# Kernel tuning notes

Measured on AMD Instinct MI355X. Metric: run time of the kernel, lower is better.

Reference implementation:

```python
import jax, jax.numpy as jnp
import numpy as np

NQ = 8
DEPTH = 2

def _apply_1q(state, U, q):
    # state: (B, 2,...,2); U: (2,2) shared or (B,2,2) per-sample; acts on qubit q
    s = jnp.moveaxis(state, 1 + q, -1)
    if U.ndim == 3:
        s = jnp.einsum('bij,b...j->b...i', U, s)
    else:
        s = jnp.einsum('ij,...j->...i', U, s)
    return jnp.moveaxis(s, -1, 1 + q)

def _cnot(state, c, t):
    s = jnp.moveaxis(state, (1 + c, 1 + t), (-2, -1))
    s = jnp.concatenate([s[..., :1, :], s[..., 1:, ::-1]], axis=-2)
    return jnp.moveaxis(s, (-2, -1), (1 + c, 1 + t))

def _rx(t):
    c = jnp.cos(t / 2).astype(jnp.complex64)
    s = (-1j * jnp.sin(t / 2)).astype(jnp.complex64)
    return jnp.stack([jnp.stack([c, s]), jnp.stack([s, c])])

def _ry(t):
    c = jnp.cos(t / 2)
    s = jnp.sin(t / 2)
    return jnp.stack([jnp.stack([c, -s]), jnp.stack([s, c])]).astype(jnp.complex64)

def _rz(t):
    e = jnp.exp(-1j * t / 2).astype(jnp.complex64)
    z = jnp.zeros((), jnp.complex64)
    return jnp.stack([jnp.stack([e, z]), jnp.stack([z, jnp.conj(e)])])

def _simulate(qparams, angles):
    # Batched 8-qubit state-vector simulator replacing the per-sample PennyLane loop.
    # angles: (B, NQ) encoding angles. qparams: (DEPTH, NQ, 3).
    B = angles.shape[0]
    state = jnp.zeros((B,) + (2,) * NQ, jnp.complex64)
    state = state.at[(slice(None),) + (0,) * NQ].set(1.0 + 0j)
    # data encoding: per-sample RX(angles[:, q]) on qubit q
    for q in range(NQ):
        t = angles[:, q]
        c = jnp.cos(t / 2).astype(jnp.complex64)
        s = (-1j * jnp.sin(t / 2)).astype(jnp.complex64)
        U = jnp.stack([jnp.stack([c, s], -1), jnp.stack([s, c], -1)], -2)  # (B,2,2)
        state = _apply_1q(state, U, q)
    for layer in range(DEPTH):
        for q in range(NQ):
            state = _apply_1q(state, _rx(qparams[layer, q, 0]), q)
            state = _apply_1q(state, _ry(qparams[layer, q, 1]), q)
            state = _apply_1q(state, _rz(qparams[layer, q, 2]), q)
        for q in range(NQ - 1):
            state = _cnot(state, q, q + 1)
    probs = state.real ** 2 + state.imag ** 2  # (B, 2,...,2)
    outs = []
    for q in range(NQ):
        axes = tuple(a for a in range(1, NQ + 1) if a != 1 + q)
        m = probs.sum(axes)  # (B, 2)
        outs.append(m[:, 0] - m[:, 1])  # <Z_q>
    return jnp.stack(outs, axis=1).astype(jnp.float32)

def _leaky(x):
    return jnp.where(x >= 0, x, 0.2 * x)

def setup_inputs():
    key = jax.random.key(0)
    k = jax.random.split(key, 16)
    B, IMG, H, NC = 4096, 128, 256, 6
    D = IMG * IMG
    def w(kk, o, i):
        return (jax.random.normal(kk, (o, i), jnp.float32) / np.float32(np.sqrt(i)))
    return {
        'img': jax.random.normal(k[0], (B, 1, IMG, IMG), jnp.float32),
        'class_id': jax.random.randint(k[1], (B,), 0, NC),
        'W1': w(k[2], H, D), 'b1': jnp.zeros((H,), jnp.float32),
        'W2': w(k[3], H, H), 'b2': jnp.zeros((H,), jnp.float32),
        'W3': w(k[4], NQ, H), 'b3': jnp.zeros((NQ,), jnp.float32),
        'qparams': jax.random.normal(k[5], (DEPTH, NQ, 3), jnp.float32),
        'emb': jax.random.normal(k[6], (NC, NC), jnp.float32),
        'W4': w(k[7], H, NQ + NC), 'b4': jnp.zeros((H,), jnp.float32),
        'W5': w(k[8], H // 2, H), 'b5': jnp.zeros((H // 2,), jnp.float32),
        'W6': w(k[9], 1, H // 2), 'b6': jnp.zeros((1,), jnp.float32),
    }

def reference(img, class_id, W1, b1, W2, b2, W3, b3, qparams, emb, W4, b4, W5, b5, W6, b6):
    B = img.shape[0]
    x = img.reshape(B, -1)
    h = _leaky(x @ W1.T + b1)
    h = _leaky(h @ W2.T + b2)
    q_in = h @ W3.T + b3  # (B, NQ)
    angles = (q_in + 1.0) * np.float32(np.pi / 2)
    # torch code wraps circuit output in torch.tensor(...) -> detached
    qf = jax.lax.stop_gradient(_simulate(qparams, angles))
    ce = emb[class_id]
    comb = jnp.concatenate([qf, ce], axis=1)
    h = _leaky(comb @ W4.T + b4)
    h = _leaky(h @ W5.T + b5)
    return h @ W6.T + b6
```

## Files before the change

### kernel.cpp

```cpp
#include <hip/hip_runtime.h>
#include <hip/hip_bf16.h>

#define B_SZ 4096
#define DDIM 16384
#define HDIM 256
#define NQ 8

typedef __attribute__((ext_vector_type(8))) short bf16x8;
typedef __attribute__((ext_vector_type(4))) short s16x4;
typedef __attribute__((ext_vector_type(4))) float f32x4;
typedef unsigned int u32;

__device__ inline short f2bf(float f) {
    union { float f; unsigned u; } v; v.f = f;
    unsigned r = v.u + 0x7fffu + ((v.u >> 16) & 1u);
    return (short)(r >> 16);
}
__device__ inline float bf2f(short h) {
    union { unsigned u; float f; } v; v.u = ((unsigned)(unsigned short)h) << 16;
    return v.f;
}
__device__ inline float lrelu(float x) { return x >= 0.f ? x : 0.2f * x; }

__device__ inline float2 cmul(float2 a, float2 b) {
    return make_float2(a.x * b.x - a.y * b.y, a.x * b.y + a.y * b.x);
}
__device__ inline float2 cadd(float2 a, float2 b) {
    return make_float2(a.x + b.x, a.y + b.y);
}

__device__ inline void async16(void* lds, const void* g) {
    __builtin_amdgcn_global_load_lds(
        (const __attribute__((address_space(1))) u32*)g,
        (__attribute__((address_space(3))) u32*)lds, 16, 0, 0);
}

__device__ inline void mk_hilo(float4 a, float4 b, bf16x8& hi, bf16x8& lo) {
    float xs[8] = {a.x, a.y, a.z, a.w, b.x, b.y, b.z, b.w};
#pragma unroll
    for (int j = 0; j < 8; j++) {
        short h = f2bf(xs[j]);
        hi[j] = h;
        lo[j] = f2bf(xs[j] - bf2f(h));
    }
}

__global__ __launch_bounds__(256) void convW(
    const float* __restrict__ W1, const float* __restrict__ W2,
    const float* __restrict__ W4, const float* __restrict__ W5,
    const float* __restrict__ qp,
    char* __restrict__ W1s, char* __restrict__ W2s,
    short* __restrict__ W4h, short* __restrict__ W4l,
    short* __restrict__ W5h, short* __restrict__ W5l,
    float* __restrict__ Umat)
{
    const int bid = blockIdx.x, t = threadIdx.x;
    if (bid < 4096) {
        int idx = bid * 256 + t;
        int r = idx >> 12, cg = idx & 4095;
        int kb = cg >> 4, c4 = cg & 15;
        float4 v = *(const float4*)(W1 + ((size_t)idx << 2));
        s16x4 h = (s16x4){f2bf(v.x), f2bf(v.y), f2bf(v.z), f2bf(v.w)};
        int byte = (r * 128 + c4 * 8) ^ ((r & 7) << 4);
        *(s16x4*)(W1s + kb * 32768 + byte) = h;
    } else if (bid < 4160) {
        int idx = (bid - 4096) * 256 + t;
        int r = idx >> 6, cg = idx & 63;
        int kb = cg >> 4, c4 = cg & 15;
        float4 v = *(const float4*)(W2 + ((size_t)idx << 2));
        s16x4 h = (s16x4){f2bf(v.x), f2bf(v.y), f2bf(v.z), f2bf(v.w)};
        int byte = (r * 128 + c4 * 8) ^ ((r & 7) << 4);
        *(s16x4*)(W2s + kb * 32768 + byte) = h;
    } else if (bid < 4192) {
        int idx = (bid - 4160) * 256 + t;
        float4 v = *(const float4*)(W5 + ((size_t)idx << 2));
        float xs[4] = {v.x, v.y, v.z, v.w};
        s16x4 hi, lo;
#pragma unroll
        for (int j = 0; j < 4; j++) {
            short h = f2bf(xs[j]);
            hi[j] = h;
            lo[j] = f2bf(xs[j] - bf2f(h));
        }
        *(s16x4*)(W5h + (size_t)idx * 4) = hi;
        *(s16x4*)(W5l + (size_t)idx * 4) = lo;
    } else {
        const float* wr = W4 + t * 14;
        short* dh = W4h + t * 32;
        short* dl = W4l + t * 32;
#pragma unroll
        for (int j = 0; j < 14; j++) {
            float x = wr[j];
            short h = f2bf(x);
            dh[j] = h;
            dl[j] = f2bf(x - bf2f(h));
        }
#pragma unroll
        for (int j = 14; j < 32; j++) { dh[j] = 0; dl[j] = 0; }
        if (t < 16) {
            float ax = qp[t * 3 + 0], ay = qp[t * 3 + 1], az = qp[t * 3 + 2];
            float sa, ca, sb, cb, sg, cg;
            sincosf(ax * 0.5f, &sa, &ca);
            sincosf(ay * 0.5f, &sb, &cb);
            sincosf(az * 0.5f, &sg, &cg);
            float2 M00 = make_float2(cb * ca,  sb * sa);
            float2 M01 = make_float2(-sb * ca, -cb * sa);
            float2 M10 = make_float2(sb * ca,  -cb * sa);
            float2 M11 = make_float2(cb * ca,  -sb * sa);
            float2 e0 = make_float2(cg, -sg);
            float2 e1 = make_float2(cg,  sg);
            float2* out = (float2*)(Umat + t * 8);
            out[0] = cmul(e0, M00);
            out[1] = cmul(e0, M01);
            out[2] = cmul(e1, M10);
            out[3] = cmul(e1, M11);
        }
    }
}

__global__ __launch_bounds__(512, 2) void gemm1(
    const float* __restrict__ img, const char* __restrict__ W1s,
    float* __restrict__ part)
{
    __shared__ char smem[2][49152];

    const int bid = blockIdx.x;
    const int y = bid & 7, x = bid >> 3;
    const int m0 = x * 128;
    const int t = threadIdx.x, lane = t & 63, w = t >> 6;
    const int arow = t >> 4, ac4 = t & 15;

    f32x4 acc[16];
#pragma unroll
    for (int i = 0; i < 16; i++) acc[i] = (f32x4){0.f, 0.f, 0.f, 0.f};
    float4 ra[4];

    const float* aBase = img + (size_t)m0 * DDIM + y * 2048;
    const char*  bBase = W1s + (size_t)(y * 32) * 32768;

    auto loadA = [&](int it) {
#pragma unroll
        for (int i = 0; i < 4; i++)
            ra[i] = *(const float4*)(aBase + (size_t)(arow + 32 * i) * DDIM + it * 64 + ac4 * 4);
    };
    auto issueB = [&](int it, int buf) {
        const char* src = bBase + it * 32768 + w * 4096 + lane * 16;
        char* dst = &smem[buf][16384 + w * 4096];
#pragma unroll
        for (int i = 0; i < 4; i++)
            async16(dst + i * 1024, src + i * 1024);
    };
    auto writeA = [&](int buf) {
#pragma unroll
        for (int i = 0; i < 4; i++) {
            int row = arow + 32 * i;
            float4 v = ra[i];
            s16x4 h = (s16x4){f2bf(v.x), f2bf(v.y), f2bf(v.z), f2bf(v.w)};
            int byte = (row * 128 + ac4 * 8) ^ ((row & 7) << 4);
            *(s16x4*)(&smem[buf][byte]) = h;
        }
    };
    auto mfma_block = [&](int buf) {
        const char* aT = &smem[buf][0];
        const char* bT = &smem[buf][16384];
#pragma unroll
        for (int ks = 0; ks < 2; ks++) {
            int k0 = ks * 32 + (lane >> 4) * 8;
            int ar = w * 16 + (lane & 15);
            bf16x8 af = *(const bf16x8*)(aT + ((ar * 128 + k0 * 2) ^ ((ar & 7) << 4)));
#pragma unroll
            for (int nf = 0; nf < 16; nf++) {
                int nr = nf * 16 + (lane & 15);
                bf16x8 bfr = *(const bf16x8*)(bT + ((nr * 128 + k0 * 2) ^ ((nr & 7) << 4)));
                acc[nf] = __builtin_amdgcn_mfma_f32_16x16x32_bf16(af, bfr, acc[nf], 0, 0, 0);
            }
        }
    };

    loadA(0);
    issueB(0, 0);
    writeA(0);
    __syncthreads();
    for (int it = 0; it < 32; ++it) {
        int bc = it & 1, bn = bc ^ 1;
        if (it < 31) { loadA(it + 1); issueB(it + 1, bn); }
        mfma_block(bc);
        if (it < 31) writeA(bn);
        __syncthreads();
    }

#pragma unroll
    for (int nf = 0; nf < 16; nf++) {
        int col = nf * 16 + (lane & 15);
#pragma unroll
        for (int r = 0; r < 4; r++) {
            int row = m0 + w * 16 + (lane >> 4) * 4 + r;
            part[((size_t)y * B_SZ + row) * 256 + col] = acc[nf][r];
        }
    }
}

__global__ __launch_bounds__(512) void gemm2(
    const float* __restrict__ part, const char* __restrict__ W2s,
    const float* __restrict__ b1, const float* __restrict__ b2,
    float* __restrict__ h2)
{
    __shared__ char smem[8192 + 32768];
    char* aT = smem;
    char* bT = smem + 8192;

    const int m0 = blockIdx.x * 64;
    const int t = threadIdx.x, lane = t & 63, w = t >> 6;
    const int wq = w & 3, half = w >> 2;

    f32x4 acc[8];
#pragma unroll
    for (int i = 0; i < 8; i++) acc[i] = (f32x4){0.f, 0.f, 0.f, 0.f};

    for (int it = 0; it < 4; ++it) {
        {
            const char* src = W2s + it * 32768 + w * 4096 + lane * 16;
            char* dst = bT + w * 4096;
#pragma unroll
            for (int i = 0; i < 4; i++)
                async16(dst + i * 1024, src + i * 1024);
        }
#pragma unroll
        for (int j = 0; j < 2; j++) {
            int g = t + j * 512;
            int row = g >> 4, c4 = g & 15;
            int kg = it * 64 + c4 * 4;
            float4 s = make_float4(0.f, 0.f, 0.f, 0.f);
#pragma unroll
            for (int yy = 0; yy < 8; yy++) {
                float4 v = *(const float4*)(part + ((size_t)yy * B_SZ + m0 + row) * 256 + kg);
                s.x += v.x; s.y += v.y; s.z += v.z; s.w += v.w;
            }
            float4 bb = *(const float4*)(b1 + kg);
            s.x = lrelu(s.x + bb.x); s.y = lrelu(s.y + bb.y);
            s.z = lrelu(s.z + bb.z); s.w = lrelu(s.w + bb.w);
            s16x4 h = (s16x4){f2bf(s.x), f2bf(s.y), f2bf(s.z), f2bf(s.w)};
            int byte = (row * 128 + c4 * 8) ^ ((row & 7) << 4);
            *(s16x4*)(aT + byte) = h;
        }
        __syncthreads();
#pragma unroll
        for (int ks = 0; ks < 2; ks++) {
            int k0 = ks * 32 + (lane >> 4) * 8;
            int ar = wq * 16 + (lane & 15);
            bf16x8 af = *(const bf16x8*)(aT + ((ar * 128 + k0 * 2) ^ ((ar & 7) << 4)));
#pragma unroll
            for (int nf = 0; nf < 8; nf++) {
                int nr = half * 128 + nf * 16 + (lane & 15);
                bf16x8 bfr = *(const bf16x8*)(bT + ((nr * 128 + k0 * 2) ^ ((nr & 7) << 4)));
                acc[nf] = __builtin_amdgcn_mfma_f32_16x16x32_bf16(af, bfr, acc[nf], 0, 0, 0);
            }
        }
        __syncthreads();
    }

#pragma unroll
    for (int nf = 0; nf < 8; nf++) {
        int col = half * 128 + nf * 16 + (lane & 15);
        float bb = b2[col];
#pragma unroll
        for (int r = 0; r < 4; r++) {
            int row = m0 + wq * 16 + (lane >> 4) * 4 + r;
            h2[(size_t)row * 256 + col] = lrelu(acc[nf][r] + bb);
        }
    }
}

__global__ __launch_bounds__(256) void qsim2(
    const float* __restrict__ h2, const float* __restrict__ W3,
    const float* __restrict__ b3, const float* __restrict__ Ug,
    float* __restrict__ qf)
{
    __shared__ float w3s[8 * 256];
    __shared__ float us[16 * 8];
    __shared__ float b3s[8];
    const int t = threadIdx.x, lane = t & 63, w = t >> 6;

    for (int i = t; i < 2048; i += 256) w3s[i] = W3[i];
    if (t < 128) us[t] = Ug[t];
    if (t < 8) b3s[t] = b3[t];
    __syncthreads();

    const int b = blockIdx.x * 4 + w;
    float4 hv = *(const float4*)(h2 + (size_t)b * 256 + lane * 4);

    float ang[8];
#pragma unroll
    for (int q = 0; q < 8; q++) {
        float4 wv = *(const float4*)(w3s + q * 256 + lane * 4);
        float p = hv.x * wv.x + hv.y * wv.y + hv.z * wv.z + hv.w * wv.w;
#pragma unroll
        for (int m = 1; m < 64; m <<= 1) p += __shfl_xor(p, m, 64);
        ang[q] = (p + b3s[q] + 1.0f) * 0.78539816339744831f;
    }
    float myang = ang[0];
#pragma unroll
    for (int q = 1; q < 8; q++) if (lane == q) myang = ang[q];
    float s_ = 0.f, c_ = 0.f;
    if (lane < 8) sincosf(myang, &s_, &c_);
    float cs[8], sn[8];
#pragma unroll
    for (int q = 0; q < 8; q++) { cs[q] = __shfl(c_, q, 64); sn[q] = __shfl(s_, q, 64); }

    float mL = 1.f;
#pragma unroll
    for (int q = 0; q <= 5; q++) mL *= ((lane >> (5 - q)) & 1) ? sn[q] : cs[q];
    float mg0 = mL * cs[6] * cs[7], mg1 = mL * cs[6] * sn[7];
    float mg2 = mL * sn[6] * cs[7], mg3 = mL * sn[6] * sn[7];
    int pc = __popc(lane);
    auto ph = [](int k, float m) {
        k &= 3;
        if (k == 0) return make_float2(m, 0.f);
        if (k == 1) return make_float2(0.f, -m);
        if (k == 2) return make_float2(-m, 0.f);
        return make_float2(0.f, m);
    };
    float2 a0 = ph(pc, mg0), a1 = ph(pc + 1, mg1), a2 = ph(pc + 1, mg2), a3 = ph(pc + 2, mg3);

#pragma unroll
    for (int l = 0; l < 2; l++) {
#pragma unroll
        for (int q = 0; q < 8; q++) {
            const float* u = us + (l * 8 + q) * 8;
            float2 u00 = make_float2(u[0], u[1]), u01 = make_float2(u[2], u[3]);
            float2 u10 = make_float2(u[4], u[5]), u11 = make_float2(u[6], u[7]);
            if (q <= 5) {
                int sh = 5 - q, msk = 1 << sh, bit = (lane >> sh) & 1;
                float2 ud = bit ? u11 : u00, uo = bit ? u10 : u01;
                float2 p;
                p.x = __shfl_xor(a0.x, msk, 64); p.y = __shfl_xor(a0.y, msk, 64);
                a0 = cadd(cmul(ud, a0), cmul(uo, p));
                p.x = __shfl_xor(a1.x, msk, 64); p.y = __shfl_xor(a1.y, msk, 64);
                a1 = cadd(cmul(ud, a1), cmul(uo, p));
                p.x = __shfl_xor(a2.x, msk, 64); p.y = __shfl_xor(a2.y, msk, 64);
                a2 = cadd(cmul(ud, a2), cmul(uo, p));
                p.x = __shfl_xor(a3.x, msk, 64); p.y = __shfl_xor(a3.y, msk, 64);
                a3 = cadd(cmul(ud, a3), cmul(uo, p));
            } else if (q == 6) {
                float2 n0 = cadd(cmul(u00, a0), cmul(u01, a2));
                float2 n2 = cadd(cmul(u10, a0), cmul(u11, a2));
                float2 n1 = cadd(cmul(u00, a1), cmul(u01, a3));
                float2 n3 = cadd(cmul(u10, a1), cmul(u11, a3));
                a0 = n0; a1 = n1; a2 = n2; a3 = n3;
            } else {
                float2 n0 = cadd(cmul(u00, a0), cmul(u01, a1));
                float2 n1 = cadd(cmul(u10, a0), cmul(u11, a1));
                float2 n2 = cadd(cmul(u00, a2), cmul(u01, a3));
                float2 n3 = cadd(cmul(u10, a2), cmul(u11, a3));
                a0 = n0; a1 = n1; a2 = n2; a3 = n3;
            }
        }
#pragma unroll
        for (int c = 0; c <= 4; c++) {
            int tm = 1 << (4 - c);
            int cb = (lane >> (5 - c)) & 1;
            float2 p;
            p.x = __shfl_xor(a0.x, tm, 64); p.y = __shfl_xor(a0.y, tm, 64);
            if (cb) a0 = p;
            p.x = __shfl_xor(a1.x, tm, 64); p.y = __shfl_xor(a1.y, tm, 64);
            if (cb) a1 = p;
            p.x = __shfl_xor(a2.x, tm, 64); p.y = __shfl_xor(a2.y, tm, 64);
            if (cb) a2 = p;
            p.x = __shfl_xor(a3.x, tm, 64); p.y = __shfl_xor(a3.y, tm, 64);
            if (cb) a3 = p;
        }
        if (lane & 1) { float2 tmp = a0; a0 = a2; a2 = tmp; tmp = a1; a1 = a3; a3 = tmp; }
        { float2 tmp = a2; a2 = a3; a3 = tmp; }
    }

    float p0 = a0.x * a0.x + a0.y * a0.y, p1 = a1.x * a1.x + a1.y * a1.y;
    float p2 = a2.x * a2.x + a2.y * a2.y, p3 = a3.x * a3.x + a3.y * a3.y;
    float S = p0 + p1 + p2 + p3;
    float v0 = ((lane >> 5) & 1) ? -S : S;
    float v1 = ((lane >> 4) & 1) ? -S : S;
    float v2 = ((lane >> 3) & 1) ? -S : S;
    float v3 = ((lane >> 2) & 1) ? -S : S;
    float v4 = ((lane >> 1) & 1) ? -S : S;
    float v5 = (lane & 1) ? -S : S;
    float v6 = p0 + p1 - p2 - p3;
    float v7 = p0 - p1 + p2 - p3;
#pragma unroll
    for (int m = 1; m < 64; m <<= 1) {
        v0 += __shfl_xor(v0, m, 64); v1 += __shfl_xor(v1, m, 64);
        v2 += __shfl_xor(v2, m, 64); v3 += __shfl_xor(v3, m, 64);
        v4 += __shfl_xor(v4, m, 64); v5 += __shfl_xor(v5, m, 64);
        v6 += __shfl_xor(v6, m, 64); v7 += __shfl_xor(v7, m, 64);
    }
    if (lane == 0) {
        float* o = qf + (size_t)b * 8;
        o[0] = v0; o[1] = v1; o[2] = v2; o[3] = v3;
        o[4] = v4; o[5] = v5; o[6] = v6; o[7] = v7;
    }
}

__global__ __launch_bounds__(256) void head_mfma(
    const float* __restrict__ qf, const int* __restrict__ cid,
    const float* __restrict__ emb,
    const short* __restrict__ W4h, const short* __restrict__ W4l,
    const float* __restrict__ b4,
    const short* __restrict__ W5h, const short* __restrict__ W5l,
    const float* __restrict__ b5,
    const float* __restrict__ W6, const float* __restrict__ b6,
    float* __restrict__ out)
{
    __shared__ float comb[64 * 32];
    __shared__ float h3s[64 * 256];
    const int t = threadIdx.x, lane = t & 63, w = t >> 6;
    const int m0 = blockIdx.x * 64;

    if (t < 128) {
        int r = t >> 1, half = t & 1;
        float* d = comb + r * 32;
        if (half == 0) {
            float4 q0 = *(const float4*)(qf + (size_t)(m0 + r) * 8);
            float4 q1 = *(const float4*)(qf + (size_t)(m0 + r) * 8 + 4);
            d[0] = q0.x; d[1] = q0.y; d[2] = q0.z; d[3] = q0.w;
            d[4] = q1.x; d[5] = q1.y; d[6] = q1.z; d[7] = q1.w;
#pragma unroll
            for (int j = 16; j < 24; j++) d[j] = 0.f;
        } else {
            const float* e = emb + cid[m0 + r] * 6;
#pragma unroll
            for (int j = 0; j < 6; j++) d[8 + j] = e[j];
            d[14] = 0.f; d[15] = 0.f;
#pragma unroll
            for (int j = 24; j < 32; j++) d[j] = 0.f;
        }
    }
    __syncthreads();

    f32x4 acc1[16];
#pragma unroll
    for (int i = 0; i < 16; i++) acc1[i] = (f32x4){0.f, 0.f, 0.f, 0.f};
    const int k0 = (lane >> 4) * 8;
    bf16x8 Ahi, Alo;
    {
        const float* p = comb + (w * 16 + (lane & 15)) * 32 + k0;
        mk_hilo(*(const float4*)p, *(const float4*)(p + 4), Ahi, Alo);
    }
#pragma unroll
    for (int nf = 0; nf < 16; nf++) {
        int n = nf * 16 + (lane & 15);
        bf16x8 Bhi = *(const bf16x8*)(W4h + n * 32 + k0);
        bf16x8 Blo = *(const bf16x8*)(W4l + n * 32 + k0);
        acc1[nf] = __builtin_amdgcn_mfma_f32_16x16x32_bf16(Ahi, Bhi, acc1[nf], 0, 0, 0);
        acc1[nf] = __builtin_amdgcn_mfma_f32_16x16x32_bf16(Ahi, Blo, acc1[nf], 0, 0, 0);
        acc1[nf] = __builtin_amdgcn_mfma_f32_16x16x32_bf16(Alo, Bhi, acc1[nf], 0, 0, 0);
    }
#pragma unroll
    for (int nf = 0; nf < 16; nf++) {
        int col = nf * 16 + (lane & 15);
        float bc = b4[col];
#pragma unroll
        for (int r = 0; r < 4; r++) {
            int row = w * 16 + (lane >> 4) * 4 + r;
            float v = lrelu(acc1[nf][r] + bc);
            int byte = row * 1024 + col * 4;
            *(float*)((char*)h3s + (byte ^ ((row & 7) << 4))) = v;
        }
    }
    __syncthreads();

    f32x4 acc2[8];
#pragma unroll
    for (int i = 0; i < 8; i++) acc2[i] = (f32x4){0.f, 0.f, 0.f, 0.f};
#pragma unroll
    for (int ks = 0; ks < 8; ks++) {
        int kf = ks * 32 + (lane >> 4) * 8;
        int row = w * 16 + (lane & 15);
        int base = row * 1024 + kf * 4;
        float4 x0 = *(float4*)((char*)h3s + (base ^ ((row & 7) << 4)));
        float4 x1 = *(float4*)((char*)h3s + ((base + 16) ^ ((row & 7) << 4)));
        bf16x8 Ah, Al;
        mk_hilo(x0, x1, Ah, Al);
#pragma unroll
        for (int nf = 0; nf < 8; nf++) {
            int n = nf * 16 + (lane & 15);
            bf16x8 Bh = *(const bf16x8*)(W5h + n * 256 + kf);
            bf16x8 Bl = *(const bf16x8*)(W5l + n * 256 + kf);
            acc2[nf] = __builtin_amdgcn_mfma_f32_16x16x32_bf16(Ah, Bh, acc2[nf], 0, 0, 0);
            acc2[nf] = __builtin_amdgcn_mfma_f32_16x16x32_bf16(Ah, Bl, acc2[nf], 0, 0, 0);
            acc2[nf] = __builtin_amdgcn_mfma_f32_16x16x32_bf16(Al, Bh, acc2[nf], 0, 0, 0);
        }
    }

    float vs0 = 0.f, vs1 = 0.f, vs2 = 0.f, vs3 = 0.f;
#pragma unroll
    for (int nf = 0; nf < 8; nf++) {
        int col = nf * 16 + (lane & 15);
        float b5c = b5[col], w6c = W6[col];
        vs0 += lrelu(acc2[nf][0] + b5c) * w6c;
        vs1 += lrelu(acc2[nf][1] + b5c) * w6c;
        vs2 += lrelu(acc2[nf][2] + b5c) * w6c;
        vs3 += lrelu(acc2[nf][3] + b5c) * w6c;
    }
#pragma unroll
    for (int m = 1; m < 16; m <<= 1) {
        vs0 += __shfl_xor(vs0, m, 64); vs1 += __shfl_xor(vs1, m, 64);
        vs2 += __shfl_xor(vs2, m, 64); vs3 += __shfl_xor(vs3, m, 64);
    }
    if ((lane & 15) == 0) {
        float bb = b6[0];
        int row = m0 + w * 16 + (lane >> 4) * 4;
        out[row + 0] = vs0 + bb;
        out[row + 1] = vs1 + bb;
        out[row + 2] = vs2 + bb;
        out[row + 3] = vs3 + bb;
    }
}

extern "C" void kernel_launch(void* const* d_in, const int* in_sizes, int n_in,
                              void* d_out, int out_size, void* d_ws, size_t ws_size,
                              hipStream_t stream)
{
    const float* img = (const float*)d_in[0];
    const int*   cid = (const int*)d_in[1];
    const float* W1  = (const float*)d_in[2];
    const float* b1  = (const float*)d_in[3];
    const float* W2  = (const float*)d_in[4];
    const float* b2  = (const float*)d_in[5];
    const float* W3  = (const float*)d_in[6];
    const float* b3  = (const float*)d_in[7];
    const float* qp  = (const float*)d_in[8];
    const float* emb = (const float*)d_in[9];
    const float* W4  = (const float*)d_in[10];
    const float* b4  = (const float*)d_in[11];
    const float* W5  = (const float*)d_in[12];
    const float* b5  = (const float*)d_in[13];
    const float* W6  = (const float*)d_in[14];
    const float* b6  = (const float*)d_in[15];

    char* ws = (char*)d_ws;
    float* part  = (float*)(ws + 0);
    float* h2    = (float*)(ws + 33554432);
    float* qfbuf = (float*)(ws + 37748736);
    float* Umat  = (float*)(ws + 37879808);
    char*  W1s   = ws + 37880320;
    char*  W2s   = ws + 46268928;
    short* W4h   = (short*)(ws + 46400000);
    short* W4l   = (short*)(ws + 46416384);
    short* W5h   = (short*)(ws + 46432768);
    short* W5l   = (short*)(ws + 46498304);

    convW<<<4193, 256, 0, stream>>>(W1, W2, W4, W5, qp,
                                    W1s, W2s, W4h, W4l, W5h, W5l, Umat);
    gemm1<<<256, 512, 0, stream>>>(img, W1s, part);
    gemm2<<<64, 512, 0, stream>>>(part, W2s, b1, b2, h2);
    qsim2<<<B_SZ / 4, 256, 0, stream>>>(h2, W3, b3, Umat, qfbuf);
    head_mfma<<<B_SZ / 64, 256, 0, stream>>>(qfbuf, cid, emb,
                                             W4h, W4l, b4, W5h, W5l, b5,
                                             W6, b6, (float*)d_out);
}
```

Baseline: 491.1 us.

## Restructure gemm1 to per-wave A tiles and direct global B-fragment loads

gemm1 now uses 256-thread blocks of 64 rows, and each wave stages its own 16-row A tile in a private LDS double buffer. B fragments are read straight from global memory (relying on cache) instead of being async-copied into shared memory. All __syncthreads are removed and A is prefetched two iterations ahead. This cuts LDS footprint and block-level synchronisation. In exchange, every wave re-reads the full B tile from global/L2, which raises cache traffic, and B loads now sit on the MFMA critical path with no LDS staging.

```diff
diff --git a/kernel.cpp b/kernel.cpp
--- a/kernel.cpp
+++ b/kernel.cpp
@@ -118,75 +118,68 @@
     }
 }
 
-__global__ __launch_bounds__(512, 2) void gemm1(
+__global__ __launch_bounds__(256, 2) void gemm1(
     const float* __restrict__ img, const char* __restrict__ W1s,
     float* __restrict__ part)
 {
-    __shared__ char smem[2][49152];
+    __shared__ char aT[4][2][2048];
 
     const int bid = blockIdx.x;
     const int y = bid & 7, x = bid >> 3;
-    const int m0 = x * 128;
+    const int m0 = x * 64;
     const int t = threadIdx.x, lane = t & 63, w = t >> 6;
-    const int arow = t >> 4, ac4 = t & 15;
 
     f32x4 acc[16];
 #pragma unroll
     for (int i = 0; i < 16; i++) acc[i] = (f32x4){0.f, 0.f, 0.f, 0.f};
+
+    const int arow = lane >> 2;
+    const int acol = lane & 3;
+    const float* aBase = img + (size_t)(m0 + w * 16 + arow) * DDIM + y * 2048;
+    const char*  bBase = W1s + (size_t)(y * 32) * 32768;
+
     float4 ra[4];
-
-    const float* aBase = img + (size_t)m0 * DDIM + y * 2048;
-    const char*  bBase = W1s + (size_t)(y * 32) * 32768;
-
     auto loadA = [&](int it) {
 #pragma unroll
-        for (int i = 0; i < 4; i++)
-            ra[i] = *(const float4*)(aBase + (size_t)(arow + 32 * i) * DDIM + it * 64 + ac4 * 4);
-    };
-    auto issueB = [&](int it, int buf) {
-        const char* src = bBase + it * 32768 + w * 4096 + lane * 16;
-        char* dst = &smem[buf][16384 + w * 4096];
-#pragma unroll
-        for (int i = 0; i < 4; i++)
-            async16(dst + i * 1024, src + i * 1024);
+        for (int j = 0; j < 4; j++)
+            ra[j] = *(const float4*)(aBase + it * 64 + (j * 4 + acol) * 4);
     };
     auto writeA = [&](int buf) {
 #pragma unroll
-        for (int i = 0; i < 4; i++) {
-            int row = arow + 32 * i;
-            float4 v = ra[i];
+        for (int j = 0; j < 4; j++) {
+            float4 v = ra[j];
             s16x4 h = (s16x4){f2bf(v.x), f2bf(v.y), f2bf(v.z), f2bf(v.w)};
-            int byte = (row * 128 + ac4 * 8) ^ ((row & 7) << 4);
-            *(s16x4*)(&smem[buf][byte]) = h;
+            int byte = (arow * 128 + (j * 4 + acol) * 8) ^ ((arow & 7) << 4);
+            *(s16x4*)(&aT[w][buf][byte]) = h;
         }
     };
-    auto mfma_block = [&](int buf) {
-        const char* aT = &smem[buf][0];
-        const char* bT = &smem[buf][16384];
+    auto mfma_block = [&](int it, int buf) {
+        const char* bIt = bBase + it * 32768;
 #pragma unroll
         for (int ks = 0; ks < 2; ks++) {
             int k0 = ks * 32 + (lane >> 4) * 8;
-            int ar = w * 16 + (lane & 15);
-            bf16x8 af = *(const bf16x8*)(aT + ((ar * 128 + k0 * 2) ^ ((ar & 7) << 4)));
+            int ar = lane & 15;
+            bf16x8 af = *(const bf16x8*)(
+                &aT[w][buf][(ar * 128 + k0 * 2) ^ ((ar & 7) << 4)]);
 #pragma unroll
             for (int nf = 0; nf < 16; nf++) {
                 int nr = nf * 16 + (lane & 15);
-                bf16x8 bfr = *(const bf16x8*)(bT + ((nr * 128 + k0 * 2) ^ ((nr & 7) << 4)));
-                acc[nf] = __builtin_amdgcn_mfma_f32_16x16x32_bf16(af, bfr, acc[nf], 0, 0, 0);
+                bf16x8 bfv = *(const bf16x8*)(
+                    bIt + ((nr * 128 + k0 * 2) ^ ((nr & 7) << 4)));
+                acc[nf] = __builtin_amdgcn_mfma_f32_16x16x32_bf16(af, bfv, acc[nf], 0, 0, 0);
             }
         }
     };
 
     loadA(0);
-    issueB(0, 0);
     writeA(0);
-    __syncthreads();
+    loadA(1);
     for (int it = 0; it < 32; ++it) {
-        int bc = it & 1, bn = bc ^ 1;
-        if (it < 31) { loadA(it + 1); issueB(it + 1, bn); }
-        mfma_block(bc);
-        if (it < 31) writeA(bn);
-        __syncthreads();
+        mfma_block(it, it & 1);
+        if (it < 31) {
+            writeA((it + 1) & 1);
+            if (it < 30) loadA(it + 2);
+        }
     }
 
 #pragma unroll
@@ -549,7 +542,7 @@
 
     convW<<<4193, 256, 0, stream>>>(W1, W2, W4, W5, qp,
                                     W1s, W2s, W4h, W4l, W5h, W5l, Umat);
-    gemm1<<<256, 512, 0, stream>>>(img, W1s, part);
+    gemm1<<<512, 256, 0, stream>>>(img, W1s, part);
     gemm2<<<64, 512, 0, stream>>>(part, W2s, b1, b2, h2);
     qsim2<<<B_SZ / 4, 256, 0, stream>>>(h2, W3, b3, Umat, qfbuf);
     head_mfma<<<B_SZ / 64, 256, 0, stream>>>(qfbuf, cid, emb,
```

Result: slower. 651.0 us (+32.5%).
